# Optimization experiments

Measured on AMD Instinct MI355X. Metric: run time of the kernel, lower is better.

The kernel has to match this reference:

```python
import jax, jax.numpy as jnp
import numpy as np

B, T, D = 4, 4096, 1024
LN_EPS = 1e-5

def _xavier(key, shape, gain=1.0):
    fan_in, fan_out = shape[1], shape[0]
    a = gain * np.sqrt(6.0 / (fan_in + fan_out))
    return jax.random.uniform(key, shape, jnp.float32, -a, a)

def setup_inputs() -> dict:
    key = jax.random.key(0)
    kx, kg, kv, ko = jax.random.split(key, 4)
    # log_decay param init so that softplus(log_decay) == decay_init (0.01)
    log_decay = jnp.asarray(np.log(np.expm1(0.01)), jnp.float32)
    return {
        "x": jax.random.normal(kx, (B, T, D), jnp.float32),
        "ln_w": jnp.ones((D,), jnp.float32),
        "ln_b": jnp.zeros((D,), jnp.float32),
        "gate_w": _xavier(kg, (D, D)),            # torch Linear weight [out, in]
        "gate_b": jnp.zeros((D,), jnp.float32),
        "value_w": _xavier(kv, (D, D), gain=0.01),
        "value_b": jnp.zeros((D,), jnp.float32),
        "out_w": _xavier(ko, (D, D), gain=0.01),
        "out_b": jnp.zeros((D,), jnp.float32),
        "log_decay": log_decay,
    }

def reference(x, ln_w, ln_b, gate_w, gate_b, value_w, value_b, out_w, out_b, log_decay):
    # LayerNorm over last dim
    mu = jnp.mean(x, axis=-1, keepdims=True)
    var = jnp.mean(jnp.square(x - mu), axis=-1, keepdims=True)
    normed = (x - mu) * jax.lax.rsqrt(var + LN_EPS) * ln_w + ln_b
    # gate / value projections (torch Linear: y = x @ W.T + b)
    g = jax.nn.sigmoid(normed @ gate_w.T + gate_b)
    v = normed @ value_w.T + value_b
    # push-pull: cumsum(g*v) - cumsum((1-g)*v) == cumsum((2g-1)*v)
    cumsum = jnp.cumsum((2.0 * g - 1.0) * v, axis=1)
    alpha = jax.nn.softplus(log_decay)
    positions = jnp.arange(T, dtype=jnp.float32)
    decay = jnp.exp(-alpha * positions)[None, :, None]  # [1, T, 1]
    output = cumsum * decay
    return x + (output @ out_w.T + out_b)
```

## Files before the change

### kernel.cpp

```cpp
#include <hip/hip_runtime.h>
#include <hip/hip_bf16.h>

#define BB 4
#define TT 4096
#define DD 1024
#define MM (BB * TT)
#define LN_EPS 1e-5f

#define NC 64
#define CL 64

typedef __attribute__((ext_vector_type(8))) short bf16x8;
typedef __attribute__((ext_vector_type(4))) float f32x4;

__device__ __forceinline__ float bfbits2f(unsigned short h) {
    return __uint_as_float(((unsigned int)h) << 16);
}
__device__ __forceinline__ unsigned short f2bfbits(float f) {
    __hip_bfloat16 h = __float2bfloat16(f);
    return *reinterpret_cast<unsigned short*>(&h);
}
__device__ __forceinline__ unsigned int pack2(float a, float b) {
    return (unsigned int)f2bfbits(a) | ((unsigned int)f2bfbits(b) << 16);
}

__device__ __forceinline__ void async_copy16(void* lds, const void* g) {
    __builtin_amdgcn_global_load_lds(
        (const __attribute__((address_space(1))) void*)g,
        (__attribute__((address_space(3))) void*)lds,
        16, 0, 0);
}

__global__ __launch_bounds__(256)
void convert_w3(const float* __restrict__ s0, const float* __restrict__ s1,
                const float* __restrict__ s2,
                __hip_bfloat16* __restrict__ d0, __hip_bfloat16* __restrict__ d1,
                __hip_bfloat16* __restrict__ d2)
{
    const int blk = blockIdx.x;
    const int w = blk >> 10;
    const float* src = (w == 0) ? s0 : (w == 1) ? s1 : s2;
    __hip_bfloat16* dst = (w == 0) ? d0 : (w == 1) ? d1 : d2;
    const size_t i = ((size_t)(blk & 1023) * 256 + threadIdx.x) * 4;
    float4 v = *(const float4*)(src + i);
    uint2 o;
    o.x = pack2(v.x, v.y);
    o.y = pack2(v.z, v.w);
    *(uint2*)((unsigned short*)dst + i) = o;
}

__global__ __launch_bounds__(256)
void ln_kernel(const float* __restrict__ x,
               const float* __restrict__ w,
               const float* __restrict__ b,
               __hip_bfloat16* __restrict__ out)
{
    const int wv   = threadIdx.x >> 6;
    const int lane = threadIdx.x & 63;
    const int row  = blockIdx.x * 4 + wv;

    const float* xr = x + (size_t)row * DD + lane * 16;
    float4 v[4];
    #pragma unroll
    for (int i = 0; i < 4; ++i) v[i] = *(const float4*)(xr + i * 4);

    float s = 0.0f, ss = 0.0f;
    #pragma unroll
    for (int i = 0; i < 4; ++i) {
        s  += (v[i].x + v[i].y) + (v[i].z + v[i].w);
        ss += fmaf(v[i].x, v[i].x, fmaf(v[i].y, v[i].y,
              fmaf(v[i].z, v[i].z, v[i].w * v[i].w)));
    }
    #pragma unroll
    for (int o = 32; o > 0; o >>= 1) {
        s  += __shfl_down(s, o);
        ss += __shfl_down(ss, o);
    }
    s  = __shfl(s, 0);
    ss = __shfl(ss, 0);

    const float mu   = s * (1.0f / DD);
    const float var  = ss * (1.0f / DD) - mu * mu;
    const float rstd = rsqrtf(var + LN_EPS);

    unsigned int res[8];
    #pragma unroll
    for (int i = 0; i < 4; ++i) {
        float4 wr = *(const float4*)(w + lane * 16 + i * 4);
        float4 br = *(const float4*)(b + lane * 16 + i * 4);
        float o0 = (v[i].x - mu) * rstd * wr.x + br.x;
        float o1 = (v[i].y - mu) * rstd * wr.y + br.y;
        float o2 = (v[i].z - mu) * rstd * wr.z + br.z;
        float o3 = (v[i].w - mu) * rstd * wr.w + br.w;
        res[i * 2]     = pack2(o0, o1);
        res[i * 2 + 1] = pack2(o2, o3);
    }
    unsigned short* op = (unsigned short*)out + (size_t)row * DD + lane * 16;
    *(uint4*)op       = make_uint4(res[0], res[1], res[2], res[3]);
    *(uint4*)(op + 8) = make_uint4(res[4], res[5], res[6], res[7]);
}

__global__ __launch_bounds__(256, 2)
void dual_gemm_gate(const __hip_bfloat16* __restrict__ A,
                    const __hip_bfloat16* __restrict__ Wg,
                    const __hip_bfloat16* __restrict__ Wv,
                    const float* __restrict__ gb,
                    const float* __restrict__ vb,
                    __hip_bfloat16* __restrict__ U,
                    float* __restrict__ Pk,
                    int M, int N, int K)
{
    constexpr int BK = 64;
    __shared__ short As[128 * BK];
    __shared__ short Bg[128 * BK];
    __shared__ short Bv[128 * BK];

    const int tid  = threadIdx.x;
    const int m0   = blockIdx.x * 128;
    const int n0   = blockIdx.y * 128;
    const int wave = tid >> 6;
    const int lane = tid & 63;
    const int wm   = (wave & 1) * 64;
    const int wn   = (wave >> 1) * 64;
    const int lrow = lane & 15;
    const int kgrp = lane >> 4;
    const int swz  = lrow & 7;

    f32x4 accg[4][4] = {};
    f32x4 accv[4][4] = {};

    const __hip_bfloat16* gA[4];
    const __hip_bfloat16* gG[4];
    const __hip_bfloat16* gV[4];
    #pragma unroll
    for (int r = 0; r < 4; ++r) {
        const int slot = r * 256 + tid;
        const int srow = slot >> 3;
        const int gcc  = (slot & 7) ^ (srow & 7);
        gA[r] = A  + (size_t)(m0 + srow) * K + gcc * 8;
        gG[r] = Wg + (size_t)(n0 + srow) * K + gcc * 8;
        gV[r] = Wv + (size_t)(n0 + srow) * K + gcc * 8;
    }

    for (int k0 = 0; k0 < K; k0 += BK) {
        #pragma unroll
        for (int r = 0; r < 4; ++r) {
            async_copy16(&As[(r * 256 + tid) * 8], gA[r] + k0);
            async_copy16(&Bg[(r * 256 + tid) * 8], gG[r] + k0);
            async_copy16(&Bv[(r * 256 + tid) * 8], gV[r] + k0);
        }
        __builtin_amdgcn_s_waitcnt(0);
        __syncthreads();

        #pragma unroll
        for (int ks = 0; ks < 2; ++ks) {
            const int co = ((ks * 4 + kgrp) ^ swz) * 8;
            bf16x8 af[4], bgf[4], bvf[4];
            #pragma unroll
            for (int i = 0; i < 4; ++i)
                af[i] = *(const bf16x8*)&As[(wm + i * 16 + lrow) * BK + co];
            #pragma unroll
            for (int j = 0; j < 4; ++j) {
                bgf[j] = *(const bf16x8*)&Bg[(wn + j * 16 + lrow) * BK + co];
                bvf[j] = *(const bf16x8*)&Bv[(wn + j * 16 + lrow) * BK + co];
            }
            #pragma unroll
            for (int i = 0; i < 4; ++i)
                #pragma unroll
                for (int j = 0; j < 4; ++j) {
                    accg[i][j] = __builtin_amdgcn_mfma_f32_16x16x32_bf16(
                        bgf[j], af[i], accg[i][j], 0, 0, 0);
                    accv[i][j] = __builtin_amdgcn_mfma_f32_16x16x32_bf16(
                        bvf[j], af[i], accv[i][j], 0, 0, 0);
                }
        }
        __syncthreads();
    }

    const int chrow = m0 + wm;
    const int cb    = chrow >> 12;
    const int cc    = (chrow & (TT - 1)) >> 6;

    #pragma unroll
    for (int j = 0; j < 4; ++j) {
        const int nb = n0 + wn + j * 16 + kgrp * 4;
        const float4 gb4 = *(const float4*)(gb + nb);
        const float4 vb4 = *(const float4*)(vb + nb);
        float4 ps = make_float4(0.f, 0.f, 0.f, 0.f);
        #pragma unroll
        for (int i = 0; i < 4; ++i) {
            const int m = m0 + wm + i * 16 + lrow;
            const float g0 = accg[i][j][0] + gb4.x, v0 = accv[i][j][0] + vb4.x;
            const float g1 = accg[i][j][1] + gb4.y, v1 = accv[i][j][1] + vb4.y;
            const float g2 = accg[i][j][2] + gb4.z, v2 = accv[i][j][2] + vb4.z;
            const float g3 = accg[i][j][3] + gb4.w, v3 = accv[i][j][3] + vb4.w;
            const float u0 = (2.0f / (1.0f + __expf(-g0)) - 1.0f) * v0;
            const float u1 = (2.0f / (1.0f + __expf(-g1)) - 1.0f) * v1;
            const float u2 = (2.0f / (1.0f + __expf(-g2)) - 1.0f) * v2;
            const float u3 = (2.0f / (1.0f + __expf(-g3)) - 1.0f) * v3;
            ps.x += u0; ps.y += u1; ps.z += u2; ps.w += u3;
            uint2 o;
            o.x = pack2(u0, u1);
            o.y = pack2(u2, u3);
            *(uint2*)((unsigned short*)U + (size_t)m * N + nb) = o;
        }
        #pragma unroll
        for (int mk = 1; mk <= 8; mk <<= 1) {
            ps.x += __shfl_xor(ps.x, mk);
            ps.y += __shfl_xor(ps.y, mk);
            ps.z += __shfl_xor(ps.z, mk);
            ps.w += __shfl_xor(ps.w, mk);
        }
        if (lrow == 0)
            *(float4*)&Pk[((size_t)cb * NC + cc) * DD + nb] = ps;
    }
}

__global__ __launch_bounds__(256, 2)
void gemm_out(const __hip_bfloat16* __restrict__ A,
              const __hip_bfloat16* __restrict__ W,
              const float* __restrict__ bias,
              const float* __restrict__ X,
              float* __restrict__ C,
              int M, int N, int K)
{
    constexpr int BK = 64;
    __shared__ short As[128 * BK];
    __shared__ short Bs[128 * BK];

    const int tid  = threadIdx.x;
    const int m0   = blockIdx.x * 128;
    const int n0   = blockIdx.y * 128;
    const int wave = tid >> 6;
    const int lane = tid & 63;
    const int wm   = (wave & 1) * 64;
    const int wn   = (wave >> 1) * 64;
    const int lrow = lane & 15;
    const int kgrp = lane >> 4;
    const int swz  = lrow & 7;

    f32x4 acc[4][4] = {};

    const __hip_bfloat16* gA[4];
    const __hip_bfloat16* gB[4];
    #pragma unroll
    for (int r = 0; r < 4; ++r) {
        const int slot = r * 256 + tid;
        const int srow = slot >> 3;
        const int gcc  = (slot & 7) ^ (srow & 7);
        gA[r] = A + (size_t)(m0 + srow) * K + gcc * 8;
        gB[r] = W + (size_t)(n0 + srow) * K + gcc * 8;
    }

    for (int k0 = 0; k0 < K; k0 += BK) {
        #pragma unroll
        for (int r = 0; r < 4; ++r) {
            async_copy16(&As[(r * 256 + tid) * 8], gA[r] + k0);
            async_copy16(&Bs[(r * 256 + tid) * 8], gB[r] + k0);
        }
        __builtin_amdgcn_s_waitcnt(0);
        __syncthreads();

        #pragma unroll
        for (int ks = 0; ks < 2; ++ks) {
            const int co = ((ks * 4 + kgrp) ^ swz) * 8;
            bf16x8 af[4], bfr[4];
            #pragma unroll
            for (int i = 0; i < 4; ++i)
                af[i] = *(const bf16x8*)&As[(wm + i * 16 + lrow) * BK + co];
            #pragma unroll
            for (int j = 0; j < 4; ++j)
                bfr[j] = *(const bf16x8*)&Bs[(wn + j * 16 + lrow) * BK + co];
            #pragma unroll
            for (int i = 0; i < 4; ++i)
                #pragma unroll
                for (int j = 0; j < 4; ++j)
                    acc[i][j] = __builtin_amdgcn_mfma_f32_16x16x32_bf16(
                        bfr[j], af[i], acc[i][j], 0, 0, 0);
        }
        __syncthreads();
    }

    #pragma unroll
    for (int j = 0; j < 4; ++j) {
        const int nb = n0 + wn + j * 16 + kgrp * 4;
        const float4 bv = *(const float4*)(bias + nb);
        #pragma unroll
        for (int i = 0; i < 4; ++i) {
            const int m = m0 + wm + i * 16 + lrow;
            const size_t idx = (size_t)m * N + nb;
            const float4 xv = *(const float4*)(X + idx);
            float4 o;
            o.x = acc[i][j][0] + bv.x + xv.x;
            o.y = acc[i][j][1] + bv.y + xv.y;
            o.z = acc[i][j][2] + bv.z + xv.z;
            o.w = acc[i][j][3] + bv.w + xv.w;
            *(float4*)(C + idx) = o;
        }
    }
}

__global__ __launch_bounds__(256)
void scan_offsets(float* __restrict__ Pk)
{
    __shared__ float Tl[64][68];
    __shared__ float Seg[4][64];

    const int tid  = threadIdx.x;
    const int col0 = blockIdx.x * 64;
    const int b    = col0 >> 10;
    const int d0   = col0 & 1023;

    #pragma unroll
    for (int r = 0; r < 4; ++r) {
        const int idx = r * 256 + tid;
        const int c = idx >> 4, q = idx & 15;
        float4 v = *(const float4*)&Pk[((size_t)b * NC + c) * DD + d0 + q * 4];
        *(float4*)&Tl[c][q * 4] = v;
    }
    __syncthreads();

    const int j = tid & 63, seg = tid >> 6;
    float ssum = 0.0f;
    #pragma unroll
    for (int k = 0; k < 16; ++k) ssum += Tl[seg * 16 + k][j];
    Seg[seg][j] = ssum;
    __syncthreads();

    float run = 0.0f;
    for (int s = 0; s < seg; ++s) run += Seg[s][j];
    #pragma unroll
    for (int k = 0; k < 16; ++k) {
        const int c = seg * 16 + k;
        const float v = Tl[c][j];
        Tl[c][j] = run;
        run += v;
    }
    __syncthreads();

    #pragma unroll
    for (int r = 0; r < 4; ++r) {
        const int idx = r * 256 + tid;
        const int c = idx >> 4, q = idx & 15;
        *(float4*)&Pk[((size_t)b * NC + c) * DD + d0 + q * 4] =
            *(const float4*)&Tl[c][q * 4];
    }
}

__global__ __launch_bounds__(128)
void scan_final(const __hip_bfloat16* __restrict__ U,
                const float* __restrict__ Pk,
                const float* __restrict__ log_decay,
                __hip_bfloat16* __restrict__ S)
{
    const int c = blockIdx.x, b = blockIdx.y;
    const int d8 = threadIdx.x * 8;

    const float ld = log_decay[0];
    const float alpha = log1pf(__expf(ld));
    const float ratio = __expf(-alpha);
    float dec = __expf(-alpha * (float)(c * CL));

    const float* pk = &Pk[((size_t)b * NC + c) * DD + d8];
    float run[8];
    float4 r0 = *(const float4*)pk;
    float4 r1 = *(const float4*)(pk + 4);
    run[0] = r0.x; run[1] = r0.y; run[2] = r0.z; run[3] = r0.w;
    run[4] = r1.x; run[5] = r1.y; run[6] = r1.z; run[7] = r1.w;

    const size_t base = ((size_t)b * TT + (size_t)c * CL) * DD + d8;
    const unsigned short* up = (const unsigned short*)U + base;
    unsigned short* sp = (unsigned short*)S + base;

    #pragma unroll 8
    for (int t = 0; t < CL; ++t) {
        uint4 raw = *(const uint4*)(up + (size_t)t * DD);
        unsigned int wds[4] = {raw.x, raw.y, raw.z, raw.w};
        uint4 o;
        unsigned int* ow = (unsigned int*)&o;
        #pragma unroll
        for (int k = 0; k < 4; ++k) {
            run[2 * k]     += bfbits2f((unsigned short)(wds[k] & 0xFFFF));
            run[2 * k + 1] += bfbits2f((unsigned short)(wds[k] >> 16));
            ow[k] = pack2(run[2 * k] * dec, run[2 * k + 1] * dec);
        }
        *(uint4*)(sp + (size_t)t * DD) = o;
        dec *= ratio;
    }
}

extern "C" void kernel_launch(void* const* d_in, const int* in_sizes, int n_in,
                              void* d_out, int out_size, void* d_ws, size_t ws_size,
                              hipStream_t stream)
{
    const float* x        = (const float*)d_in[0];
    const float* ln_w     = (const float*)d_in[1];
    const float* ln_b     = (const float*)d_in[2];
    const float* gate_w   = (const float*)d_in[3];
    const float* gate_b   = (const float*)d_in[4];
    const float* value_w  = (const float*)d_in[5];
    const float* value_b  = (const float*)d_in[6];
    const float* out_w    = (const float*)d_in[7];
    const float* out_b    = (const float*)d_in[8];
    const float* log_dec  = (const float*)d_in[9];
    float* out = (float*)d_out;

    char* ws = (char*)d_ws;
    const size_t MB = 1024 * 1024;
    __hip_bfloat16* normed = (__hip_bfloat16*)(ws);
    __hip_bfloat16* S      = (__hip_bfloat16*)(ws);
    float*          Pk     = (float*)(ws + 32 * MB);
    __hip_bfloat16* Wg16   = (__hip_bfloat16*)(ws + 33 * MB);
    __hip_bfloat16* Wv16   = (__hip_bfloat16*)(ws + 35 * MB);
    __hip_bfloat16* Wo16   = (__hip_bfloat16*)(ws + 37 * MB);
    __hip_bfloat16* U      = (__hip_bfloat16*)d_out;

    convert_w3<<<dim3(3072), dim3(256), 0, stream>>>(
        gate_w, value_w, out_w, Wg16, Wv16, Wo16);

    ln_kernel<<<dim3(MM / 4), dim3(256), 0, stream>>>(x, ln_w, ln_b, normed);

    dual_gemm_gate<<<dim3(MM / 128, DD / 128), dim3(256), 0, stream>>>(
        normed, Wg16, Wv16, gate_b, value_b, U, Pk, MM, DD, DD);

    scan_offsets<<<dim3(NC), dim3(256), 0, stream>>>(Pk);
    scan_final<<<dim3(NC, BB), dim3(128), 0, stream>>>(U, Pk, log_dec, S);

    gemm_out<<<dim3(MM / 128, DD / 128), dim3(256), 0, stream>>>(
        S, Wo16, out_b, x, out, MM, DD, DD);
}
```

Before: 291.4 us.

## Triple-buffer GEMM K-loops with 512-thread blocks and larger output tile

Both GEMM kernels replace the load-wait-compute loop with a three-stage LDS ring. Tiles two steps ahead are prefetched with async copies, and a partial vmcnt wait plus a barrier replace the full drain each step. Blocks grow to 8 waves: the dual gate/value GEMM splits N more finely per wave, and the output GEMM moves to a 256x128 tile. s_setprio is raised around the MFMA bursts. The ring buffers use about 144KB of LDS, which likely limits each CU to one block and trades occupancy for overlap of loads and compute.

```diff
diff --git a/kernel.cpp b/kernel.cpp
--- a/kernel.cpp
+++ b/kernel.cpp
@@ -100,7 +100,7 @@
     *(uint4*)(op + 8) = make_uint4(res[4], res[5], res[6], res[7]);
 }
 
-__global__ __launch_bounds__(256, 2)
+__global__ __launch_bounds__(512, 2)
 void dual_gemm_gate(const __hip_bfloat16* __restrict__ A,
                     const __hip_bfloat16* __restrict__ Wg,
                     const __hip_bfloat16* __restrict__ Wv,
@@ -111,9 +111,8 @@
                     int M, int N, int K)
 {
     constexpr int BK = 64;
-    __shared__ short As[128 * BK];
-    __shared__ short Bg[128 * BK];
-    __shared__ short Bv[128 * BK];
+    constexpr int NT = DD / BK;
+    __shared__ short ring[3][3][128 * BK];
 
     const int tid  = threadIdx.x;
     const int m0   = blockIdx.x * 128;
@@ -121,20 +120,20 @@
     const int wave = tid >> 6;
     const int lane = tid & 63;
     const int wm   = (wave & 1) * 64;
-    const int wn   = (wave >> 1) * 64;
+    const int wn   = (wave >> 1) * 32;
     const int lrow = lane & 15;
     const int kgrp = lane >> 4;
     const int swz  = lrow & 7;
 
-    f32x4 accg[4][4] = {};
-    f32x4 accv[4][4] = {};
-
-    const __hip_bfloat16* gA[4];
-    const __hip_bfloat16* gG[4];
-    const __hip_bfloat16* gV[4];
-    #pragma unroll
-    for (int r = 0; r < 4; ++r) {
-        const int slot = r * 256 + tid;
+    f32x4 accg[4][2] = {};
+    f32x4 accv[4][2] = {};
+
+    const __hip_bfloat16* gA[2];
+    const __hip_bfloat16* gG[2];
+    const __hip_bfloat16* gV[2];
+    #pragma unroll
+    for (int r = 0; r < 2; ++r) {
+        const int slot = r * 512 + tid;
         const int srow = slot >> 3;
         const int gcc  = (slot & 7) ^ (srow & 7);
         gA[r] = A  + (size_t)(m0 + srow) * K + gcc * 8;
@@ -142,39 +141,58 @@
         gV[r] = Wv + (size_t)(n0 + srow) * K + gcc * 8;
     }
 
-    for (int k0 = 0; k0 < K; k0 += BK) {
-        #pragma unroll
-        for (int r = 0; r < 4; ++r) {
-            async_copy16(&As[(r * 256 + tid) * 8], gA[r] + k0);
-            async_copy16(&Bg[(r * 256 + tid) * 8], gG[r] + k0);
-            async_copy16(&Bv[(r * 256 + tid) * 8], gV[r] + k0);
-        }
-        __builtin_amdgcn_s_waitcnt(0);
-        __syncthreads();
-
+    auto stage = [&](int sbuf, int kofs) {
+        #pragma unroll
+        for (int r = 0; r < 2; ++r) {
+            const int so = (r * 512 + tid) * 8;
+            async_copy16(&ring[sbuf][0][so], gA[r] + kofs);
+            async_copy16(&ring[sbuf][1][so], gG[r] + kofs);
+            async_copy16(&ring[sbuf][2][so], gV[r] + kofs);
+        }
+    };
+
+    stage(0, 0);
+    stage(1, BK);
+    asm volatile("s_waitcnt vmcnt(6)\n\ts_barrier" ::: "memory");
+
+    int rb = 0, sb = 2;
+    for (int t = 0; t < NT; ++t) {
+        if (t < NT - 2) stage(sb, (t + 2) * BK);
+
+        const short* As = ring[rb][0];
+        const short* Bg = ring[rb][1];
+        const short* Bv = ring[rb][2];
         #pragma unroll
         for (int ks = 0; ks < 2; ++ks) {
             const int co = ((ks * 4 + kgrp) ^ swz) * 8;
-            bf16x8 af[4], bgf[4], bvf[4];
+            bf16x8 af[4], bgf[2], bvf[2];
             #pragma unroll
             for (int i = 0; i < 4; ++i)
                 af[i] = *(const bf16x8*)&As[(wm + i * 16 + lrow) * BK + co];
             #pragma unroll
-            for (int j = 0; j < 4; ++j) {
+            for (int j = 0; j < 2; ++j) {
                 bgf[j] = *(const bf16x8*)&Bg[(wn + j * 16 + lrow) * BK + co];
                 bvf[j] = *(const bf16x8*)&Bv[(wn + j * 16 + lrow) * BK + co];
             }
+            __builtin_amdgcn_s_setprio(1);
             #pragma unroll
             for (int i = 0; i < 4; ++i)
                 #pragma unroll
-                for (int j = 0; j < 4; ++j) {
+                for (int j = 0; j < 2; ++j) {
                     accg[i][j] = __builtin_amdgcn_mfma_f32_16x16x32_bf16(
                         bgf[j], af[i], accg[i][j], 0, 0, 0);
                     accv[i][j] = __builtin_amdgcn_mfma_f32_16x16x32_bf16(
                         bvf[j], af[i], accv[i][j], 0, 0, 0);
                 }
-        }
-        __syncthreads();
+            __builtin_amdgcn_s_setprio(0);
+        }
+
+        if (t < NT - 2)
+            asm volatile("s_waitcnt vmcnt(6)\n\ts_barrier" ::: "memory");
+        else if (t == NT - 2)
+            asm volatile("s_waitcnt vmcnt(0)\n\ts_barrier" ::: "memory");
+        rb = (rb == 2) ? 0 : rb + 1;
+        sb = (sb == 2) ? 0 : sb + 1;
     }
 
     const int chrow = m0 + wm;
@@ -182,7 +200,7 @@
     const int cc    = (chrow & (TT - 1)) >> 6;
 
     #pragma unroll
-    for (int j = 0; j < 4; ++j) {
+    for (int j = 0; j < 2; ++j) {
         const int nb = n0 + wn + j * 16 + kgrp * 4;
         const float4 gb4 = *(const float4*)(gb + nb);
         const float4 vb4 = *(const float4*)(vb + nb);
@@ -216,7 +234,7 @@
     }
 }
 
-__global__ __launch_bounds__(256, 2)
+__global__ __launch_bounds__(512, 2)
 void gemm_out(const __hip_bfloat16* __restrict__ A,
               const __hip_bfloat16* __restrict__ W,
               const float* __restrict__ bias,
@@ -225,16 +243,17 @@
               int M, int N, int K)
 {
     constexpr int BK = 64;
-    __shared__ short As[128 * BK];
-    __shared__ short Bs[128 * BK];
+    constexpr int NT = DD / BK;
+    __shared__ short As_[3][256 * BK];
+    __shared__ short Bs_[3][128 * BK];
 
     const int tid  = threadIdx.x;
-    const int m0   = blockIdx.x * 128;
+    const int m0   = blockIdx.x * 256;
     const int n0   = blockIdx.y * 128;
     const int wave = tid >> 6;
     const int lane = tid & 63;
-    const int wm   = (wave & 1) * 64;
-    const int wn   = (wave >> 1) * 64;
+    const int wm   = (wave & 3) * 64;
+    const int wn   = (wave >> 2) * 64;
     const int lrow = lane & 15;
     const int kgrp = lane >> 4;
     const int swz  = lrow & 7;
@@ -242,25 +261,41 @@
     f32x4 acc[4][4] = {};
 
     const __hip_bfloat16* gA[4];
-    const __hip_bfloat16* gB[4];
+    const __hip_bfloat16* gB[2];
     #pragma unroll
     for (int r = 0; r < 4; ++r) {
-        const int slot = r * 256 + tid;
+        const int slot = r * 512 + tid;
         const int srow = slot >> 3;
         const int gcc  = (slot & 7) ^ (srow & 7);
         gA[r] = A + (size_t)(m0 + srow) * K + gcc * 8;
+    }
+    #pragma unroll
+    for (int r = 0; r < 2; ++r) {
+        const int slot = r * 512 + tid;
+        const int srow = slot >> 3;
+        const int gcc  = (slot & 7) ^ (srow & 7);
         gB[r] = W + (size_t)(n0 + srow) * K + gcc * 8;
     }
 
-    for (int k0 = 0; k0 < K; k0 += BK) {
-        #pragma unroll
-        for (int r = 0; r < 4; ++r) {
-            async_copy16(&As[(r * 256 + tid) * 8], gA[r] + k0);
-            async_copy16(&Bs[(r * 256 + tid) * 8], gB[r] + k0);
-        }
-        __builtin_amdgcn_s_waitcnt(0);
-        __syncthreads();
-
+    auto stage = [&](int sbuf, int kofs) {
+        #pragma unroll
+        for (int r = 0; r < 4; ++r)
+            async_copy16(&As_[sbuf][(r * 512 + tid) * 8], gA[r] + kofs);
+        #pragma unroll
+        for (int r = 0; r < 2; ++r)
+            async_copy16(&Bs_[sbuf][(r * 512 + tid) * 8], gB[r] + kofs);
+    };
+
+    stage(0, 0);
+    stage(1, BK);
+    asm volatile("s_waitcnt vmcnt(6)\n\ts_barrier" ::: "memory");
+
+    int rb = 0, sb = 2;
+    for (int t = 0; t < NT; ++t) {
+        if (t < NT - 2) stage(sb, (t + 2) * BK);
+
+        const short* As = As_[rb];
+        const short* Bs = Bs_[rb];
         #pragma unroll
         for (int ks = 0; ks < 2; ++ks) {
             const int co = ((ks * 4 + kgrp) ^ swz) * 8;
@@ -271,14 +306,22 @@
             #pragma unroll
             for (int j = 0; j < 4; ++j)
                 bfr[j] = *(const bf16x8*)&Bs[(wn + j * 16 + lrow) * BK + co];
+            __builtin_amdgcn_s_setprio(1);
             #pragma unroll
             for (int i = 0; i < 4; ++i)
                 #pragma unroll
                 for (int j = 0; j < 4; ++j)
                     acc[i][j] = __builtin_amdgcn_mfma_f32_16x16x32_bf16(
                         bfr[j], af[i], acc[i][j], 0, 0, 0);
-        }
-        __syncthreads();
+            __builtin_amdgcn_s_setprio(0);
+        }
+
+        if (t < NT - 2)
+            asm volatile("s_waitcnt vmcnt(6)\n\ts_barrier" ::: "memory");
+        else if (t == NT - 2)
+            asm volatile("s_waitcnt vmcnt(0)\n\ts_barrier" ::: "memory");
+        rb = (rb == 2) ? 0 : rb + 1;
+        sb = (sb == 2) ? 0 : sb + 1;
     }
 
     #pragma unroll
@@ -420,12 +463,12 @@
 
     ln_kernel<<<dim3(MM / 4), dim3(256), 0, stream>>>(x, ln_w, ln_b, normed);
 
-    dual_gemm_gate<<<dim3(MM / 128, DD / 128), dim3(256), 0, stream>>>(
+    dual_gemm_gate<<<dim3(MM / 128, DD / 128), dim3(512), 0, stream>>>(
         normed, Wg16, Wv16, gate_b, value_b, U, Pk, MM, DD, DD);
 
     scan_offsets<<<dim3(NC), dim3(256), 0, stream>>>(Pk);
     scan_final<<<dim3(NC, BB), dim3(128), 0, stream>>>(U, Pk, log_dec, S);
 
-    gemm_out<<<dim3(MM / 128, DD / 128), dim3(256), 0, stream>>>(
+    gemm_out<<<dim3(MM / 256, DD / 128), dim3(512), 0, stream>>>(
         S, Wo16, out_b, x, out, MM, DD, DD);
 }
```

After: 302.2 us. +3.7%, slower.

## Merge weight-convert with layernorm and fold chunk-offset scan into final scan

Applied to the files above, without the earlier changes.

Weight bf16 conversion and layernorm now run in one launch, split by block index. The separate scan_offsets kernel is removed. scan_final now uses 1024 threads per chunk, with 8 waves-groups each owning 8 timesteps. Each block sums the preceding chunk totals from Pk itself and combines per-group partial sums through LDS. This removes two launches and gives the sequential 64-step scan more parallelism. In exchange, each block redundantly reads up to 63 chunk-sum rows and uses 64KB of LDS.

```diff
diff --git a/kernel.cpp b/kernel.cpp
--- a/kernel.cpp
+++ b/kernel.cpp
@@ -32,32 +32,31 @@
 }
 
 __global__ __launch_bounds__(256)
-void convert_w3(const float* __restrict__ s0, const float* __restrict__ s1,
-                const float* __restrict__ s2,
-                __hip_bfloat16* __restrict__ d0, __hip_bfloat16* __restrict__ d1,
-                __hip_bfloat16* __restrict__ d2)
+void prep_kernel(const float* __restrict__ s0, const float* __restrict__ s1,
+                 const float* __restrict__ s2,
+                 __hip_bfloat16* __restrict__ d0, __hip_bfloat16* __restrict__ d1,
+                 __hip_bfloat16* __restrict__ d2,
+                 const float* __restrict__ x,
+                 const float* __restrict__ lnw,
+                 const float* __restrict__ lnb,
+                 __hip_bfloat16* __restrict__ normed)
 {
-    const int blk = blockIdx.x;
-    const int w = blk >> 10;
-    const float* src = (w == 0) ? s0 : (w == 1) ? s1 : s2;
-    __hip_bfloat16* dst = (w == 0) ? d0 : (w == 1) ? d1 : d2;
-    const size_t i = ((size_t)(blk & 1023) * 256 + threadIdx.x) * 4;
-    float4 v = *(const float4*)(src + i);
-    uint2 o;
-    o.x = pack2(v.x, v.y);
-    o.y = pack2(v.z, v.w);
-    *(uint2*)((unsigned short*)dst + i) = o;
-}
-
-__global__ __launch_bounds__(256)
-void ln_kernel(const float* __restrict__ x,
-               const float* __restrict__ w,
-               const float* __restrict__ b,
-               __hip_bfloat16* __restrict__ out)
-{
+    if (blockIdx.x < 3072) {
+        const int blk = blockIdx.x;
+        const int w = blk >> 10;
+        const float* src = (w == 0) ? s0 : (w == 1) ? s1 : s2;
+        __hip_bfloat16* dst = (w == 0) ? d0 : (w == 1) ? d1 : d2;
+        const size_t i = ((size_t)(blk & 1023) * 256 + threadIdx.x) * 4;
+        float4 v = *(const float4*)(src + i);
+        uint2 o;
+        o.x = pack2(v.x, v.y);
+        o.y = pack2(v.z, v.w);
+        *(uint2*)((unsigned short*)dst + i) = o;
+        return;
+    }
     const int wv   = threadIdx.x >> 6;
     const int lane = threadIdx.x & 63;
-    const int row  = blockIdx.x * 4 + wv;
+    const int row  = (blockIdx.x - 3072) * 4 + wv;
 
     const float* xr = x + (size_t)row * DD + lane * 16;
     float4 v[4];
@@ -86,8 +85,8 @@
     unsigned int res[8];
     #pragma unroll
     for (int i = 0; i < 4; ++i) {
-        float4 wr = *(const float4*)(w + lane * 16 + i * 4);
-        float4 br = *(const float4*)(b + lane * 16 + i * 4);
+        float4 wr = *(const float4*)(lnw + lane * 16 + i * 4);
+        float4 br = *(const float4*)(lnb + lane * 16 + i * 4);
         float o0 = (v[i].x - mu) * rstd * wr.x + br.x;
         float o1 = (v[i].y - mu) * rstd * wr.y + br.y;
         float o2 = (v[i].z - mu) * rstd * wr.z + br.z;
@@ -95,7 +94,7 @@
         res[i * 2]     = pack2(o0, o1);
         res[i * 2 + 1] = pack2(o2, o3);
     }
-    unsigned short* op = (unsigned short*)out + (size_t)row * DD + lane * 16;
+    unsigned short* op = (unsigned short*)normed + (size_t)row * DD + lane * 16;
     *(uint4*)op       = make_uint4(res[0], res[1], res[2], res[3]);
     *(uint4*)(op + 8) = make_uint4(res[4], res[5], res[6], res[7]);
 }
@@ -300,82 +299,75 @@
     }
 }
 
-__global__ __launch_bounds__(256)
-void scan_offsets(float* __restrict__ Pk)
-{
-    __shared__ float Tl[64][68];
-    __shared__ float Seg[4][64];
-
-    const int tid  = threadIdx.x;
-    const int col0 = blockIdx.x * 64;
-    const int b    = col0 >> 10;
-    const int d0   = col0 & 1023;
-
-    #pragma unroll
-    for (int r = 0; r < 4; ++r) {
-        const int idx = r * 256 + tid;
-        const int c = idx >> 4, q = idx & 15;
-        float4 v = *(const float4*)&Pk[((size_t)b * NC + c) * DD + d0 + q * 4];
-        *(float4*)&Tl[c][q * 4] = v;
-    }
-    __syncthreads();
-
-    const int j = tid & 63, seg = tid >> 6;
-    float ssum = 0.0f;
-    #pragma unroll
-    for (int k = 0; k < 16; ++k) ssum += Tl[seg * 16 + k][j];
-    Seg[seg][j] = ssum;
-    __syncthreads();
-
-    float run = 0.0f;
-    for (int s = 0; s < seg; ++s) run += Seg[s][j];
-    #pragma unroll
-    for (int k = 0; k < 16; ++k) {
-        const int c = seg * 16 + k;
-        const float v = Tl[c][j];
-        Tl[c][j] = run;
-        run += v;
-    }
-    __syncthreads();
-
-    #pragma unroll
-    for (int r = 0; r < 4; ++r) {
-        const int idx = r * 256 + tid;
-        const int c = idx >> 4, q = idx & 15;
-        *(float4*)&Pk[((size_t)b * NC + c) * DD + d0 + q * 4] =
-            *(const float4*)&Tl[c][q * 4];
-    }
-}
-
-__global__ __launch_bounds__(128)
+__global__ __launch_bounds__(1024)
 void scan_final(const __hip_bfloat16* __restrict__ U,
                 const float* __restrict__ Pk,
                 const float* __restrict__ log_decay,
                 __hip_bfloat16* __restrict__ S)
 {
-    const int c = blockIdx.x, b = blockIdx.y;
-    const int d8 = threadIdx.x * 8;
-
-    const float ld = log_decay[0];
+    __shared__ float LdsC[8][DD];
+    __shared__ float LdsP[8][DD];
+
+    const int c  = blockIdx.x, b = blockIdx.y;
+    const int w  = threadIdx.x >> 7;
+    const int dg = threadIdx.x & 127;
+    const int d8 = dg * 8;
+
+    const float ld    = log_decay[0];
     const float alpha = log1pf(__expf(ld));
     const float ratio = __expf(-alpha);
-    float dec = __expf(-alpha * (float)(c * CL));
-
-    const float* pk = &Pk[((size_t)b * NC + c) * DD + d8];
-    float run[8];
-    float4 r0 = *(const float4*)pk;
-    float4 r1 = *(const float4*)(pk + 4);
-    run[0] = r0.x; run[1] = r0.y; run[2] = r0.z; run[3] = r0.w;
-    run[4] = r1.x; run[5] = r1.y; run[6] = r1.z; run[7] = r1.w;
-
-    const size_t base = ((size_t)b * TT + (size_t)c * CL) * DD + d8;
+
+    const size_t base = ((size_t)b * TT + (size_t)c * CL + w * 8) * DD + d8;
     const unsigned short* up = (const unsigned short*)U + base;
+
+    uint4 raw[8];
+    float cs[8] = {0.f, 0.f, 0.f, 0.f, 0.f, 0.f, 0.f, 0.f};
+    #pragma unroll
+    for (int r = 0; r < 8; ++r) {
+        raw[r] = *(const uint4*)(up + (size_t)r * DD);
+        const unsigned int wds[4] = {raw[r].x, raw[r].y, raw[r].z, raw[r].w};
+        #pragma unroll
+        for (int k = 0; k < 4; ++k) {
+            cs[2 * k]     += bfbits2f((unsigned short)(wds[k] & 0xFFFF));
+            cs[2 * k + 1] += bfbits2f((unsigned short)(wds[k] >> 16));
+        }
+    }
+
+    float pp[8] = {0.f, 0.f, 0.f, 0.f, 0.f, 0.f, 0.f, 0.f};
+    for (int cc = w; cc < c; cc += 8) {
+        const float* pr = &Pk[((size_t)b * NC + cc) * DD + d8];
+        const float4 a0 = *(const float4*)pr;
+        const float4 a1 = *(const float4*)(pr + 4);
+        pp[0] += a0.x; pp[1] += a0.y; pp[2] += a0.z; pp[3] += a0.w;
+        pp[4] += a1.x; pp[5] += a1.y; pp[6] += a1.z; pp[7] += a1.w;
+    }
+
+    *(float4*)&LdsC[w][d8]     = make_float4(cs[0], cs[1], cs[2], cs[3]);
+    *(float4*)&LdsC[w][d8 + 4] = make_float4(cs[4], cs[5], cs[6], cs[7]);
+    *(float4*)&LdsP[w][d8]     = make_float4(pp[0], pp[1], pp[2], pp[3]);
+    *(float4*)&LdsP[w][d8 + 4] = make_float4(pp[4], pp[5], pp[6], pp[7]);
+    __syncthreads();
+
+    float run[8] = {0.f, 0.f, 0.f, 0.f, 0.f, 0.f, 0.f, 0.f};
+    #pragma unroll
+    for (int w2 = 0; w2 < 8; ++w2) {
+        const float4 p0 = *(const float4*)&LdsP[w2][d8];
+        const float4 p1 = *(const float4*)&LdsP[w2][d8 + 4];
+        run[0] += p0.x; run[1] += p0.y; run[2] += p0.z; run[3] += p0.w;
+        run[4] += p1.x; run[5] += p1.y; run[6] += p1.z; run[7] += p1.w;
+        if (w2 < w) {
+            const float4 c0 = *(const float4*)&LdsC[w2][d8];
+            const float4 c1 = *(const float4*)&LdsC[w2][d8 + 4];
+            run[0] += c0.x; run[1] += c0.y; run[2] += c0.z; run[3] += c0.w;
+            run[4] += c1.x; run[5] += c1.y; run[6] += c1.z; run[7] += c1.w;
+        }
+    }
+
+    float dec = __expf(-alpha * (float)(c * CL + w * 8));
     unsigned short* sp = (unsigned short*)S + base;
-
-    #pragma unroll 8
-    for (int t = 0; t < CL; ++t) {
-        uint4 raw = *(const uint4*)(up + (size_t)t * DD);
-        unsigned int wds[4] = {raw.x, raw.y, raw.z, raw.w};
+    #pragma unroll
+    for (int r = 0; r < 8; ++r) {
+        const unsigned int wds[4] = {raw[r].x, raw[r].y, raw[r].z, raw[r].w};
         uint4 o;
         unsigned int* ow = (unsigned int*)&o;
         #pragma unroll
@@ -384,7 +376,7 @@
             run[2 * k + 1] += bfbits2f((unsigned short)(wds[k] >> 16));
             ow[k] = pack2(run[2 * k] * dec, run[2 * k + 1] * dec);
         }
-        *(uint4*)(sp + (size_t)t * DD) = o;
+        *(uint4*)(sp + (size_t)r * DD) = o;
         dec *= ratio;
     }
 }
@@ -415,16 +407,13 @@
     __hip_bfloat16* Wo16   = (__hip_bfloat16*)(ws + 37 * MB);
     __hip_bfloat16* U      = (__hip_bfloat16*)d_out;
 
-    convert_w3<<<dim3(3072), dim3(256), 0, stream>>>(
-        gate_w, value_w, out_w, Wg16, Wv16, Wo16);
-
-    ln_kernel<<<dim3(MM / 4), dim3(256), 0, stream>>>(x, ln_w, ln_b, normed);
+    prep_kernel<<<dim3(3072 + MM / 4), dim3(256), 0, stream>>>(
+        gate_w, value_w, out_w, Wg16, Wv16, Wo16, x, ln_w, ln_b, normed);
 
     dual_gemm_gate<<<dim3(MM / 128, DD / 128), dim3(256), 0, stream>>>(
         normed, Wg16, Wv16, gate_b, value_b, U, Pk, MM, DD, DD);
 
-    scan_offsets<<<dim3(NC), dim3(256), 0, stream>>>(Pk);
-    scan_final<<<dim3(NC, BB), dim3(128), 0, stream>>>(U, Pk, log_dec, S);
+    scan_final<<<dim3(NC, BB), dim3(1024), 0, stream>>>(U, Pk, log_dec, S);
 
     gemm_out<<<dim3(MM / 128, DD / 128), dim3(256), 0, stream>>>(
         S, Wo16, out_b, x, out, MM, DD, DD);
```

Result: faster. 282.4 us (-3.1%).
